# Optimization experiments

Measured on AMD Instinct MI355X. Metric: run time of the kernel, lower is better.

The kernel has to match this reference:

```python
import jax, jax.numpy as jnp
import numpy as np

# Config mirroring MultiHeadAttention1d(in_channels=256, n_heads=8, residual=False,
# kernel_size=1, attention_type=0) applied to 3-D inputs (B, C, N).
B, C, N, H, D = 4, 256, 2048, 8, 256  # per-head dim D = in_channels; OC = H*D = 2048
OC = H * D


def setup_inputs() -> dict:
    key = jax.random.key(0)
    ks = jax.random.split(key, 14)
    s = 1.0 / np.sqrt(C)
    f32 = jnp.float32
    inp = {
        "x": jax.random.normal(ks[0], (B, C, N), f32),
        "y": jax.random.normal(ks[1], (B, C, N), f32),
        # ConvNormActivation1d (kernel_size=1) == pointwise conv + (folded, eval-mode)
        # BatchNorm affine + ReLU. BN folds to per-channel scale g and shift beta.
        "Wq": jax.random.normal(ks[2], (OC, C), f32) * s,
        "bq": jax.random.normal(ks[3], (OC,), f32) * 0.01,
        "gq": jnp.ones((OC,), f32),
        "betaq": jnp.zeros((OC,), f32),
        "Wk": jax.random.normal(ks[4], (OC, C), f32) * s,
        "bk": jax.random.normal(ks[5], (OC,), f32) * 0.01,
        "gk": jnp.ones((OC,), f32),
        "betak": jnp.zeros((OC,), f32),
        "Wv": jax.random.normal(ks[6], (OC, C), f32) * s,
        "bv": jax.random.normal(ks[7], (OC,), f32) * 0.01,
        "gv": jnp.ones((OC,), f32),
        "betav": jnp.zeros((OC,), f32),
    }
    return inp


def _cna(W, b, g, beta, t):
    # 1x1 conv (channel GEMM) + folded-BN affine + ReLU; t: (B, C, N) -> (B, OC, N)
    z = jnp.einsum("oc,bcn->bon", W, t) + b[:, None]
    return jax.nn.relu(g[:, None] * z + beta[:, None])


def _heads(t):
    # (B, OC, N) -> (B, H, N, D); channel split matches torch.split chunks of size D
    return t.reshape(B, H, D, N).transpose(0, 1, 3, 2)


def reference(x, y, Wq, bq, gq, betaq, Wk, bk, gk, betak, Wv, bv, gv, betav):
    q = _heads(_cna(Wq, bq, gq, betaq, x))  # (B,H,N,D)
    k = _heads(_cna(Wk, bk, gk, betak, y))
    v = _heads(_cna(Wv, bv, gv, betav, y))
    energy = jnp.einsum("bhnd,bhmd->bhnm", q, k)  # bmm(Q, K^T)
    attn = jax.nn.softmax(energy, axis=-1)
    out = jnp.einsum("bhnm,bhmd->bhnd", attn, v)  # (B,H,N,D)
    # torch path: view(H,B,k,N,D).permute(1,0,3,2,4) -> (B,H,N,k=1,D);
    # squeeze(dim=2) is a no-op since N != 1.
    return out[:, :, :, None, :]  # (B, H, N, 1, D)
```

## Files before the change

### kernel.cpp

```cpp
#include <hip/hip_runtime.h>
#include <cstdint>
#include <cstddef>

typedef unsigned short u16;
typedef __attribute__((ext_vector_type(4))) float f32x4;
typedef __attribute__((ext_vector_type(8))) _Float16 f16x8;
typedef __attribute__((ext_vector_type(4))) u16   u16x4;
typedef __attribute__((ext_vector_type(8))) u16   u16x8;

#define DEV static __device__ __forceinline__
#define MFMA16(a,b,c) __builtin_amdgcn_mfma_f32_16x16x32_f16((a),(b),(c),0,0,0)

constexpr int Bc = 4, Cc = 256, Nc = 2048, Hc = 8, Dc = 256, OCc = 2048;

constexpr size_t OFF_XT = 0;
constexpr size_t OFF_YT = OFF_XT + (size_t)Bc*Nc*Cc*2;
constexpr size_t OFF_WQ = OFF_YT + (size_t)Bc*Nc*Cc*2;
constexpr size_t OFF_WK = OFF_WQ + (size_t)OCc*Cc*2;
constexpr size_t OFF_WV = OFF_WK + (size_t)OCc*Cc*2;
constexpr size_t OFF_BQ = OFF_WV + (size_t)OCc*Cc*2;
constexpr size_t OFF_BK = OFF_BQ + (size_t)OCc*4;
constexpr size_t OFF_BV = OFF_BK + (size_t)OCc*4;
constexpr size_t OFF_Q  = OFF_BV + (size_t)OCc*4;
constexpr size_t OFF_K  = OFF_Q  + (size_t)Bc*Hc*Nc*Dc*2;
constexpr size_t OFF_V  = OFF_K  + (size_t)Bc*Hc*Nc*Dc*2;

DEV u16 f2h(float x){
  _Float16 h = (_Float16)x;
  return __builtin_bit_cast(u16, h);
}

DEV void load_lds16(const void* g, void* l){
  __builtin_amdgcn_global_load_lds((const __attribute__((address_space(1))) int*)g,
                                   (__attribute__((address_space(3))) int*)l, 16, 0, 0);
}

__global__ __launch_bounds__(256) void transpose_cast(const float* __restrict__ x,
                                                      const float* __restrict__ y,
                                                      u16* __restrict__ XT,
                                                      u16* __restrict__ YT){
  __shared__ u16 tile[64][65];
  int b = blockIdx.z >> 1;
  const float* src = (blockIdx.z & 1) ? y : x;
  u16* dst = (blockIdx.z & 1) ? YT : XT;
  int n0 = blockIdx.x * 64, c0 = blockIdx.y * 64;
  int t = threadIdx.x;
#pragma unroll
  for (int i = 0; i < 16; ++i){
    int slot = i*256 + t;
    int cl = slot >> 6, nl = slot & 63;
    tile[cl][nl] = f2h(src[((size_t)b*Cc + c0 + cl)*Nc + n0 + nl]);
  }
  __syncthreads();
#pragma unroll
  for (int i = 0; i < 8; ++i){
    int slot = i*256 + t;
    int nl = slot >> 5, cl = (slot & 31)*2;
    uint32_t v = (uint32_t)tile[cl][nl] | ((uint32_t)tile[cl+1][nl] << 16);
    *(uint32_t*)(dst + ((size_t)b*Nc + n0 + nl)*Cc + c0 + cl) = v;
  }
}

__global__ __launch_bounds__(256) void prep_w(const float* __restrict__ W,
                                              const float* __restrict__ bsrc,
                                              const float* __restrict__ g,
                                              const float* __restrict__ beta,
                                              u16* __restrict__ Wo,
                                              float* __restrict__ bb){
  int idx = (blockIdx.x*256 + threadIdx.x) * 8;
  int o = idx >> 8, c = idx & 255;
  float gg = g[o];
  f32x4 a0 = *(const f32x4*)(W + idx);
  f32x4 a1 = *(const f32x4*)(W + idx + 4);
  u16x8 r;
#pragma unroll
  for (int i = 0; i < 4; ++i){ r[i] = f2h(a0[i]*gg); r[i+4] = f2h(a1[i]*gg); }
  *(u16x8*)(Wo + idx) = r;
  if (c == 0) bb[o] = gg*bsrc[o] + beta[o];
}

template<int SW>
__global__ __launch_bounds__(256, 2) void proj_gemm(const u16* __restrict__ Xt,
                                                    const u16* __restrict__ Wp,
                                                    const float* __restrict__ bb,
                                                    u16* __restrict__ outp){
  __shared__ __align__(16) char lds[32768];
  int t = threadIdx.x, w = t >> 6, l = t & 63, q = l & 15, g = l >> 4;
  int b = blockIdx.z;
  int n0 = blockIdx.x * 128, o0 = blockIdx.y * 128;
  f32x4 acc[4][4] = {};

  for (int it = 0; it < 4; ++it){
    __syncthreads();
#pragma unroll
    for (int j = 0; j < 8; ++j){
      int s = j*4 + w;
      int chunk = s >> 3;
      int off = (s & 7) * 1024;
      int row = (s & 7)*16 + (l >> 2);
      int part = l & 3;
      const char* gsrc;
      if (chunk < 2)
        gsrc = (const char*)(Wp + (size_t)(o0 + row)*Cc) + it*128 + chunk*64 + part*16;
      else
        gsrc = (const char*)(Xt + ((size_t)b*Nc + n0 + row)*Cc) + it*128 + (chunk & 1)*64 + part*16;
      load_lds16(gsrc, lds + chunk*8192 + off);
    }
    asm volatile("s_waitcnt vmcnt(0)" ::: "memory");
    __syncthreads();
#pragma unroll
    for (int kc = 0; kc < 2; ++kc){
      f16x8 fw[4], fx[4];
#pragma unroll
      for (int i = 0; i < 4; ++i){
        int wrow = (SW ? (w & 1) : (w >> 1))*64 + i*16 + q;
        int xrow = (SW ? (w >> 1) : (w & 1))*64 + i*16 + q;
        fw[i] = *(const f16x8*)(lds + kc*8192 + wrow*64 + g*16);
        fx[i] = *(const f16x8*)(lds + 16384 + kc*8192 + xrow*64 + g*16);
      }
#pragma unroll
      for (int i = 0; i < 4; ++i)
#pragma unroll
        for (int jj = 0; jj < 4; ++jj){
          if constexpr (!SW) acc[i][jj] = MFMA16(fw[i], fx[jj], acc[i][jj]);
          else               acc[i][jj] = MFMA16(fx[i], fw[jj], acc[i][jj]);
        }
    }
  }

  if constexpr (!SW) {
    f32x4 bias[4];
#pragma unroll
    for (int i = 0; i < 4; ++i) bias[i] = *(const f32x4*)(bb + o0 + (w>>1)*64 + i*16 + 4*g);
#pragma unroll
    for (int i = 0; i < 4; ++i)
#pragma unroll
      for (int jj = 0; jj < 4; ++jj){
        u16x4 pk;
#pragma unroll
        for (int r = 0; r < 4; ++r){
          float z = acc[i][jj][r] + bias[i][r];
          pk[r] = f2h(fmaxf(z, 0.f));
        }
        int o = o0 + (w>>1)*64 + i*16 + 4*g;
        int n = n0 + (w&1)*64 + jj*16 + q;
        int hh = o >> 8, d = o & 255;
        *(u16x4*)(outp + ((size_t)((b*Hc + hh)*Nc + n))*Dc + d) = pk;
      }
  } else {
    float biasv[4];
#pragma unroll
    for (int i = 0; i < 4; ++i) biasv[i] = bb[o0 + (w&1)*64 + i*16 + q];
#pragma unroll
    for (int i = 0; i < 4; ++i)
#pragma unroll
      for (int jj = 0; jj < 4; ++jj){
        u16x4 pk;
#pragma unroll
        for (int r = 0; r < 4; ++r){
          float z = acc[i][jj][r] + biasv[jj];
          pk[r] = f2h(fmaxf(z, 0.f));
        }
        int o = o0 + (w&1)*64 + jj*16 + q;
        int n = n0 + (w>>1)*64 + i*16 + 4*g;
        int hh = o >> 8, d = o & 255;
        *(u16x4*)(outp + ((size_t)((b*Hc + hh)*Dc + d))*Nc + n) = pk;
      }
  }
}

__global__ __launch_bounds__(256, 2) void attn_kernel(const u16* __restrict__ Qp,
                                                      const u16* __restrict__ Kp,
                                                      const u16* __restrict__ Vp,
                                                      float* __restrict__ outp){
  __shared__ __align__(16) char lds[32768 + 16384 + 4*2304];
  int t = threadIdx.x, w = t >> 6, l = t & 63, q = l & 15, g = l >> 4;
  int qt = blockIdx.x, h = blockIdx.y, b = blockIdx.z;
  int q0 = qt * 64;
  size_t head = (size_t)(b*Hc + h) * Nc * Dc;
  const u16* Kh = Kp + head;
  const u16* Vh = Vp + head;

  f16x8 qf[8];
  const u16* qrow = Qp + head + (size_t)(q0 + w*16 + q) * Dc;
#pragma unroll
  for (int kk = 0; kk < 8; ++kk) qf[kk] = *(const f16x8*)(qrow + kk*32 + g*8);

  f32x4 acc_o[16] = {};
  float m_run = -1e30f, l_run = 0.f;
  char* pbase = lds + 49152 + w*2304;

  for (int kv = 0; kv < 32; ++kv){
    int m0 = kv * 64;
    __syncthreads();
#pragma unroll
    for (int j = 0; j < 8; ++j){
      int row = w*16 + (l >> 2);
      const char* gsrc = (const char*)(Kh + (size_t)(m0 + row)*Dc) + j*64 + (l & 3)*16;
      load_lds16(gsrc, lds + j*4096 + w*1024);
    }
#pragma unroll
    for (int j = 0; j < 4; ++j){
      int s = j*4 + w;
      int row = s*16 + (l >> 2);
      const char* gsrc = (const char*)(Vh + (size_t)row*Nc + m0 + (l & 3)*8);
      load_lds16(gsrc, lds + 32768 + s*1024);
    }
    asm volatile("s_waitcnt vmcnt(0)" ::: "memory");
    __syncthreads();

    f32x4 s_acc[4];
#pragma unroll
    for (int mt = 0; mt < 4; ++mt){
      f32x4 a = {0.f, 0.f, 0.f, 0.f};
#pragma unroll
      for (int kk = 0; kk < 8; ++kk){
        f16x8 kf = *(const f16x8*)(lds + kk*4096 + (mt*16 + q)*64 + g*16);
        a = MFMA16(kf, qf[kk], a);
      }
      s_acc[mt] = a;
    }

    float tmax = -1e30f;
#pragma unroll
    for (int mt = 0; mt < 4; ++mt)
#pragma unroll
      for (int r = 0; r < 4; ++r) tmax = fmaxf(tmax, s_acc[mt][r]);
    tmax = fmaxf(tmax, __shfl_xor(tmax, 16));
    tmax = fmaxf(tmax, __shfl_xor(tmax, 32));
    float mnew = fmaxf(m_run, tmax);
    float scale = __expf(m_run - mnew);
    float rsum = 0.f;
#pragma unroll
    for (int mt = 0; mt < 4; ++mt){
      u16x4 pk;
#pragma unroll
      for (int r = 0; r < 4; ++r){
        float p = __expf(s_acc[mt][r] - mnew);
        rsum += p;
        pk[r] = f2h(p);
      }
      *(u16x4*)(pbase + q*144 + (mt*16 + 4*g)*2) = pk;
    }
    rsum += __shfl_xor(rsum, 16);
    rsum += __shfl_xor(rsum, 32);
    l_run = l_run * scale + rsum;
    m_run = mnew;
#pragma unroll
    for (int dt = 0; dt < 16; ++dt) acc_o[dt] *= scale;

    f16x8 pb0 = *(const f16x8*)(pbase + q*144 + g*16);
    f16x8 pb1 = *(const f16x8*)(pbase + q*144 + 64 + g*16);

#pragma unroll
    for (int dt = 0; dt < 16; ++dt){
      f16x8 vf = *(const f16x8*)(lds + 32768 + (dt*16 + q)*64 + g*16);
      acc_o[dt] = MFMA16(vf, pb0, acc_o[dt]);
    }
    __syncthreads();
#pragma unroll
    for (int j = 0; j < 4; ++j){
      int s = j*4 + w;
      int row = s*16 + (l >> 2);
      const char* gsrc = (const char*)(Vh + (size_t)row*Nc + m0 + 32 + (l & 3)*8);
      load_lds16(gsrc, lds + 32768 + s*1024);
    }
    asm volatile("s_waitcnt vmcnt(0)" ::: "memory");
    __syncthreads();
#pragma unroll
    for (int dt = 0; dt < 16; ++dt){
      f16x8 vf = *(const f16x8*)(lds + 32768 + (dt*16 + q)*64 + g*16);
      acc_o[dt] = MFMA16(vf, pb1, acc_o[dt]);
    }
  }

  float inv = 1.f / l_run;
  size_t obase = ((size_t)(b*Hc + h)*Nc + q0 + w*16 + q) * Dc;
#pragma unroll
  for (int dt = 0; dt < 16; ++dt){
    f32x4 v = acc_o[dt] * inv;
    *(f32x4*)(outp + obase + dt*16 + 4*g) = v;
  }
}

extern "C" void kernel_launch(void* const* d_in, const int* in_sizes, int n_in,
                              void* d_out, int out_size, void* d_ws, size_t ws_size,
                              hipStream_t stream){
  const float* x     = (const float*)d_in[0];
  const float* y     = (const float*)d_in[1];
  const float* Wq    = (const float*)d_in[2];
  const float* bq    = (const float*)d_in[3];
  const float* gq    = (const float*)d_in[4];
  const float* betaq = (const float*)d_in[5];
  const float* Wk    = (const float*)d_in[6];
  const float* bk    = (const float*)d_in[7];
  const float* gk    = (const float*)d_in[8];
  const float* betak = (const float*)d_in[9];
  const float* Wv    = (const float*)d_in[10];
  const float* bv    = (const float*)d_in[11];
  const float* gv    = (const float*)d_in[12];
  const float* betav = (const float*)d_in[13];
  char* ws = (char*)d_ws;
  float* outp = (float*)d_out;

  u16* XT = (u16*)(ws + OFF_XT);
  u16* YT = (u16*)(ws + OFF_YT);
  u16* WQb = (u16*)(ws + OFF_WQ);
  u16* WKb = (u16*)(ws + OFF_WK);
  u16* WVb = (u16*)(ws + OFF_WV);
  float* BQ = (float*)(ws + OFF_BQ);
  float* BK = (float*)(ws + OFF_BK);
  float* BV = (float*)(ws + OFF_BV);
  u16* Qw = (u16*)(ws + OFF_Q);
  u16* Kw = (u16*)(ws + OFF_K);
  u16* Vw = (u16*)(ws + OFF_V);

  transpose_cast<<<dim3(Nc/64, Cc/64, Bc*2), 256, 0, stream>>>(x, y, XT, YT);
  prep_w<<<dim3(OCc*Cc/2048), 256, 0, stream>>>(Wq, bq, gq, betaq, WQb, BQ);
  prep_w<<<dim3(OCc*Cc/2048), 256, 0, stream>>>(Wk, bk, gk, betak, WKb, BK);
  prep_w<<<dim3(OCc*Cc/2048), 256, 0, stream>>>(Wv, bv, gv, betav, WVb, BV);

  dim3 pg(Nc/128, OCc/128, Bc);
  proj_gemm<0><<<pg, 256, 0, stream>>>(XT, WQb, BQ, Qw);
  proj_gemm<0><<<pg, 256, 0, stream>>>(YT, WKb, BK, Kw);
  proj_gemm<1><<<pg, 256, 0, stream>>>(YT, WVb, BV, Vw);

  attn_kernel<<<dim3(Nc/64, Hc, Bc), 256, 0, stream>>>(Qw, Kw, Vw, outp);
}
```

Baseline: 304.0 us.

## Double attention query tile per wave and XOR-swizzle LDS layouts

The attention kernel now processes 128 queries per block, with each wave holding two 16-row query fragments. Every K and V fragment read from LDS therefore feeds two MFMAs, which halves K/V global and LDS traffic per query. K, V and the projection GEMM tiles are stored in LDS with XOR swizzles to cut bank conflicts on fragment reads. The cost is doubled accumulator registers (acc_o grows to 32 f32x4), which can lower occupancy or cause spills, and the block count drops by half.

Result: slower. 503.7 us (+65.7%).

```diff
diff --git a/kernel.cpp b/kernel.cpp
--- a/kernel.cpp
+++ b/kernel.cpp
@@ -88,6 +88,8 @@
   int t = threadIdx.x, w = t >> 6, l = t & 63, q = l & 15, g = l >> 4;
   int b = blockIdx.z;
   int n0 = blockIdx.x * 128, o0 = blockIdx.y * 128;
+  int fs = ((q >> 1) & 3) << 4;
+  int partg = ((l & 3) ^ ((l >> 3) & 3));
   f32x4 acc[4][4] = {};
 
   for (int it = 0; it < 4; ++it){
@@ -98,12 +100,11 @@
       int chunk = s >> 3;
       int off = (s & 7) * 1024;
       int row = (s & 7)*16 + (l >> 2);
-      int part = l & 3;
       const char* gsrc;
       if (chunk < 2)
-        gsrc = (const char*)(Wp + (size_t)(o0 + row)*Cc) + it*128 + chunk*64 + part*16;
+        gsrc = (const char*)(Wp + (size_t)(o0 + row)*Cc) + it*128 + chunk*64 + partg*16;
       else
-        gsrc = (const char*)(Xt + ((size_t)b*Nc + n0 + row)*Cc) + it*128 + (chunk & 1)*64 + part*16;
+        gsrc = (const char*)(Xt + ((size_t)b*Nc + n0 + row)*Cc) + it*128 + (chunk & 1)*64 + partg*16;
       load_lds16(gsrc, lds + chunk*8192 + off);
     }
     asm volatile("s_waitcnt vmcnt(0)" ::: "memory");
@@ -115,8 +116,8 @@
       for (int i = 0; i < 4; ++i){
         int wrow = (SW ? (w & 1) : (w >> 1))*64 + i*16 + q;
         int xrow = (SW ? (w >> 1) : (w & 1))*64 + i*16 + q;
-        fw[i] = *(const f16x8*)(lds + kc*8192 + wrow*64 + g*16);
-        fx[i] = *(const f16x8*)(lds + 16384 + kc*8192 + xrow*64 + g*16);
+        fw[i] = *(const f16x8*)(lds + kc*8192 + wrow*64 + ((g*16) ^ fs));
+        fx[i] = *(const f16x8*)(lds + 16384 + kc*8192 + xrow*64 + ((g*16) ^ fs));
       }
 #pragma unroll
       for (int i = 0; i < 4; ++i)
@@ -173,113 +174,141 @@
                                                       const u16* __restrict__ Kp,
                                                       const u16* __restrict__ Vp,
                                                       float* __restrict__ outp){
-  __shared__ __align__(16) char lds[32768 + 16384 + 4*2304];
-  int t = threadIdx.x, w = t >> 6, l = t & 63, q = l & 15, g = l >> 4;
-  int qt = blockIdx.x, h = blockIdx.y, b = blockIdx.z;
-  int q0 = qt * 64;
+  __shared__ __align__(16) char lds[32768 + 16384 + 4*4608];
+  int t = threadIdx.x, w = t >> 6, l = t & 63, q16 = l & 15, g = l >> 4;
+  int h = blockIdx.y, b = blockIdx.z;
+  int q0 = blockIdx.x * 128;
   size_t head = (size_t)(b*Hc + h) * Nc * Dc;
   const u16* Kh = Kp + head;
   const u16* Vh = Vp + head;
 
-  f16x8 qf[8];
-  const u16* qrow = Qp + head + (size_t)(q0 + w*16 + q) * Dc;
-#pragma unroll
-  for (int kk = 0; kk < 8; ++kk) qf[kk] = *(const f16x8*)(qrow + kk*32 + g*8);
-
-  f32x4 acc_o[16] = {};
-  float m_run = -1e30f, l_run = 0.f;
-  char* pbase = lds + 49152 + w*2304;
+  f16x8 qf[2][8];
+#pragma unroll
+  for (int jq = 0; jq < 2; ++jq){
+    const u16* qrow = Qp + head + (size_t)(q0 + w*32 + jq*16 + q16) * Dc;
+#pragma unroll
+    for (int kk = 0; kk < 8; ++kk) qf[jq][kk] = *(const f16x8*)(qrow + kk*32 + g*8);
+  }
+
+  f32x4 acc_o[16][2] = {};
+  float m_run[2] = {-1e30f, -1e30f}, l_run[2] = {0.f, 0.f};
+  char* pbase = lds + 49152 + w*4608;
+
+  const int swzA = (q16 & 7) << 4;
+  const int swzV = ((q16 >> 1) & 3) << 4;
+  const int gslotV = ((l & 3) ^ ((l >> 3) & 3));
 
   for (int kv = 0; kv < 32; ++kv){
     int m0 = kv * 64;
     __syncthreads();
 #pragma unroll
     for (int j = 0; j < 8; ++j){
-      int row = w*16 + (l >> 2);
-      const char* gsrc = (const char*)(Kh + (size_t)(m0 + row)*Dc) + j*64 + (l & 3)*16;
-      load_lds16(gsrc, lds + j*4096 + w*1024);
+      int ri = j*4 + w;
+      int mg = 2*ri + (l >> 5);
+      int gslot = (l & 31) ^ (mg & 7);
+      const char* gsrc = (const char*)(Kh + (size_t)(m0 + mg)*Dc + gslot*8);
+      load_lds16(gsrc, lds + ri*1024);
     }
 #pragma unroll
     for (int j = 0; j < 4; ++j){
-      int s = j*4 + w;
-      int row = s*16 + (l >> 2);
-      const char* gsrc = (const char*)(Vh + (size_t)row*Nc + m0 + (l & 3)*8);
-      load_lds16(gsrc, lds + 32768 + s*1024);
+      int ri = j*4 + w;
+      int dg = 16*ri + (l >> 2);
+      const char* gsrc = (const char*)(Vh + (size_t)dg*Nc + m0 + gslotV*8);
+      load_lds16(gsrc, lds + 32768 + ri*1024);
     }
     asm volatile("s_waitcnt vmcnt(0)" ::: "memory");
     __syncthreads();
 
-    f32x4 s_acc[4];
+    f32x4 s_acc[4][2];
 #pragma unroll
     for (int mt = 0; mt < 4; ++mt){
-      f32x4 a = {0.f, 0.f, 0.f, 0.f};
+      f32x4 a0 = {0.f,0.f,0.f,0.f}, a1 = {0.f,0.f,0.f,0.f};
 #pragma unroll
       for (int kk = 0; kk < 8; ++kk){
-        f16x8 kf = *(const f16x8*)(lds + kk*4096 + (mt*16 + q)*64 + g*16);
-        a = MFMA16(kf, qf[kk], a);
-      }
-      s_acc[mt] = a;
-    }
-
-    float tmax = -1e30f;
-#pragma unroll
-    for (int mt = 0; mt < 4; ++mt)
-#pragma unroll
-      for (int r = 0; r < 4; ++r) tmax = fmaxf(tmax, s_acc[mt][r]);
-    tmax = fmaxf(tmax, __shfl_xor(tmax, 16));
-    tmax = fmaxf(tmax, __shfl_xor(tmax, 32));
-    float mnew = fmaxf(m_run, tmax);
-    float scale = __expf(m_run - mnew);
-    float rsum = 0.f;
-#pragma unroll
-    for (int mt = 0; mt < 4; ++mt){
-      u16x4 pk;
-#pragma unroll
-      for (int r = 0; r < 4; ++r){
-        float p = __expf(s_acc[mt][r] - mnew);
-        rsum += p;
-        pk[r] = f2h(p);
-      }
-      *(u16x4*)(pbase + q*144 + (mt*16 + 4*g)*2) = pk;
-    }
-    rsum += __shfl_xor(rsum, 16);
-    rsum += __shfl_xor(rsum, 32);
-    l_run = l_run * scale + rsum;
-    m_run = mnew;
-#pragma unroll
-    for (int dt = 0; dt < 16; ++dt) acc_o[dt] *= scale;
-
-    f16x8 pb0 = *(const f16x8*)(pbase + q*144 + g*16);
-    f16x8 pb1 = *(const f16x8*)(pbase + q*144 + 64 + g*16);
-
+        f16x8 kf = *(const f16x8*)(lds + (mt*16 + q16)*512 + ((kk*64 + g*16) ^ swzA));
+        a0 = MFMA16(kf, qf[0][kk], a0);
+        a1 = MFMA16(kf, qf[1][kk], a1);
+      }
+      s_acc[mt][0] = a0; s_acc[mt][1] = a1;
+    }
+
+    float scale_[2];
+#pragma unroll
+    for (int jq = 0; jq < 2; ++jq){
+      float tmax = -1e30f;
+#pragma unroll
+      for (int mt = 0; mt < 4; ++mt)
+#pragma unroll
+        for (int r = 0; r < 4; ++r) tmax = fmaxf(tmax, s_acc[mt][jq][r]);
+      tmax = fmaxf(tmax, __shfl_xor(tmax, 16));
+      tmax = fmaxf(tmax, __shfl_xor(tmax, 32));
+      float mnew = fmaxf(m_run[jq], tmax);
+      float sc = __expf(m_run[jq] - mnew);
+      float rsum = 0.f;
+#pragma unroll
+      for (int mt = 0; mt < 4; ++mt){
+        u16x4 pk;
+#pragma unroll
+        for (int r = 0; r < 4; ++r){
+          float p = __expf(s_acc[mt][jq][r] - mnew);
+          rsum += p;
+          pk[r] = f2h(p);
+        }
+        *(u16x4*)(pbase + (jq*16 + q16)*144 + mt*32 + g*8) = pk;
+      }
+      rsum += __shfl_xor(rsum, 16);
+      rsum += __shfl_xor(rsum, 32);
+      l_run[jq] = l_run[jq]*sc + rsum;
+      m_run[jq] = mnew;
+      scale_[jq] = sc;
+    }
 #pragma unroll
     for (int dt = 0; dt < 16; ++dt){
-      f16x8 vf = *(const f16x8*)(lds + 32768 + (dt*16 + q)*64 + g*16);
-      acc_o[dt] = MFMA16(vf, pb0, acc_o[dt]);
+      acc_o[dt][0] *= scale_[0];
+      acc_o[dt][1] *= scale_[1];
+    }
+
+    {
+      f16x8 pb0 = *(const f16x8*)(pbase + (0*16 + q16)*144 + g*16);
+      f16x8 pb1 = *(const f16x8*)(pbase + (1*16 + q16)*144 + g*16);
+#pragma unroll
+      for (int dt = 0; dt < 16; ++dt){
+        f16x8 vf = *(const f16x8*)(lds + 32768 + (dt*16 + q16)*64 + ((g*16) ^ swzV));
+        acc_o[dt][0] = MFMA16(vf, pb0, acc_o[dt][0]);
+        acc_o[dt][1] = MFMA16(vf, pb1, acc_o[dt][1]);
+      }
     }
     __syncthreads();
 #pragma unroll
     for (int j = 0; j < 4; ++j){
-      int s = j*4 + w;
-      int row = s*16 + (l >> 2);
-      const char* gsrc = (const char*)(Vh + (size_t)row*Nc + m0 + 32 + (l & 3)*8);
-      load_lds16(gsrc, lds + 32768 + s*1024);
+      int ri = j*4 + w;
+      int dg = 16*ri + (l >> 2);
+      const char* gsrc = (const char*)(Vh + (size_t)dg*Nc + m0 + 32 + gslotV*8);
+      load_lds16(gsrc, lds + 32768 + ri*1024);
     }
     asm volatile("s_waitcnt vmcnt(0)" ::: "memory");
     __syncthreads();
+    {
+      f16x8 pb0 = *(const f16x8*)(pbase + (0*16 + q16)*144 + 64 + g*16);
+      f16x8 pb1 = *(const f16x8*)(pbase + (1*16 + q16)*144 + 64 + g*16);
+#pragma unroll
+      for (int dt = 0; dt < 16; ++dt){
+        f16x8 vf = *(const f16x8*)(lds + 32768 + (dt*16 + q16)*64 + ((g*16) ^ swzV));
+        acc_o[dt][0] = MFMA16(vf, pb0, acc_o[dt][0]);
+        acc_o[dt][1] = MFMA16(vf, pb1, acc_o[dt][1]);
+      }
+    }
+  }
+
+#pragma unroll
+  for (int jq = 0; jq < 2; ++jq){
+    float inv = 1.f / l_run[jq];
+    size_t obase = ((size_t)(b*Hc + h)*Nc + q0 + w*32 + jq*16 + q16) * Dc;
 #pragma unroll
     for (int dt = 0; dt < 16; ++dt){
-      f16x8 vf = *(const f16x8*)(lds + 32768 + (dt*16 + q)*64 + g*16);
-      acc_o[dt] = MFMA16(vf, pb1, acc_o[dt]);
-    }
-  }
-
-  float inv = 1.f / l_run;
-  size_t obase = ((size_t)(b*Hc + h)*Nc + q0 + w*16 + q) * Dc;
-#pragma unroll
-  for (int dt = 0; dt < 16; ++dt){
-    f32x4 v = acc_o[dt] * inv;
-    *(f32x4*)(outp + obase + dt*16 + 4*g) = v;
+      f32x4 v = acc_o[dt][jq] * inv;
+      *(f32x4*)(outp + obase + dt*16 + 4*g) = v;
+    }
   }
 }
 
@@ -325,5 +354,5 @@
   proj_gemm<0><<<pg, 256, 0, stream>>>(YT, WKb, BK, Kw);
   proj_gemm<1><<<pg, 256, 0, stream>>>(YT, WVb, BV, Vw);
 
-  attn_kernel<<<dim3(Nc/64, Hc, Bc), 256, 0, stream>>>(Qw, Kw, Vw, outp);
-}
+  attn_kernel<<<dim3(Nc/128, Hc, Bc), 256, 0, stream>>>(Qw, Kw, Vw, outp);
+}
```

## Rework attention kernel with 32x32 MFMA tiles, swizzled LDS and 2x2 wave split

Applied to the files above, without the earlier changes.

The attention kernel now splits work across a 2x2 wave grid, with each wave covering 32 queries and either half of the KV columns or half of the head dimension. It uses 32x32x16 MFMA instead of 16x16x32, and cross-wave row max, row sum and scale are exchanged through LDS. K, V and the projection GEMM tiles get XOR-swizzled LDS layouts to avoid bank conflicts. The aim is more data reuse per MFMA and fewer LDS conflicts. The cost is extra block-wide barriers per KV step and scalar, non-vectorized output stores.

Result: no change. 307.8 us (+1.2%).

```diff
diff --git a/kernel.cpp b/kernel.cpp
--- a/kernel.cpp
+++ b/kernel.cpp
@@ -4,12 +4,15 @@
 
 typedef unsigned short u16;
 typedef __attribute__((ext_vector_type(4))) float f32x4;
+typedef __attribute__((ext_vector_type(16))) float f32x16;
 typedef __attribute__((ext_vector_type(8))) _Float16 f16x8;
 typedef __attribute__((ext_vector_type(4))) u16   u16x4;
 typedef __attribute__((ext_vector_type(8))) u16   u16x8;
+typedef __attribute__((ext_vector_type(4))) int   i32x4;
 
 #define DEV static __device__ __forceinline__
 #define MFMA16(a,b,c) __builtin_amdgcn_mfma_f32_16x16x32_f16((a),(b),(c),0,0,0)
+#define MFMA32(a,b,c) __builtin_amdgcn_mfma_f32_32x32x16_f16((a),(b),(c),0,0,0)
 
 constexpr int Bc = 4, Cc = 256, Nc = 2048, Hc = 8, Dc = 256, OCc = 2048;
 
@@ -88,6 +91,8 @@
   int t = threadIdx.x, w = t >> 6, l = t & 63, q = l & 15, g = l >> 4;
   int b = blockIdx.z;
   int n0 = blockIdx.x * 128, o0 = blockIdx.y * 128;
+  int fs = ((q >> 1) & 3) << 4;
+  int partg = ((l & 3) ^ ((l >> 3) & 3));
   f32x4 acc[4][4] = {};
 
   for (int it = 0; it < 4; ++it){
@@ -98,12 +103,11 @@
       int chunk = s >> 3;
       int off = (s & 7) * 1024;
       int row = (s & 7)*16 + (l >> 2);
-      int part = l & 3;
       const char* gsrc;
       if (chunk < 2)
-        gsrc = (const char*)(Wp + (size_t)(o0 + row)*Cc) + it*128 + chunk*64 + part*16;
+        gsrc = (const char*)(Wp + (size_t)(o0 + row)*Cc) + it*128 + chunk*64 + partg*16;
       else
-        gsrc = (const char*)(Xt + ((size_t)b*Nc + n0 + row)*Cc) + it*128 + (chunk & 1)*64 + part*16;
+        gsrc = (const char*)(Xt + ((size_t)b*Nc + n0 + row)*Cc) + it*128 + (chunk & 1)*64 + partg*16;
       load_lds16(gsrc, lds + chunk*8192 + off);
     }
     asm volatile("s_waitcnt vmcnt(0)" ::: "memory");
@@ -115,8 +119,8 @@
       for (int i = 0; i < 4; ++i){
         int wrow = (SW ? (w & 1) : (w >> 1))*64 + i*16 + q;
         int xrow = (SW ? (w >> 1) : (w & 1))*64 + i*16 + q;
-        fw[i] = *(const f16x8*)(lds + kc*8192 + wrow*64 + g*16);
-        fx[i] = *(const f16x8*)(lds + 16384 + kc*8192 + xrow*64 + g*16);
+        fw[i] = *(const f16x8*)(lds + kc*8192 + wrow*64 + ((g*16) ^ fs));
+        fx[i] = *(const f16x8*)(lds + 16384 + kc*8192 + xrow*64 + ((g*16) ^ fs));
       }
 #pragma unroll
       for (int i = 0; i < 4; ++i)
@@ -173,114 +177,154 @@
                                                       const u16* __restrict__ Kp,
                                                       const u16* __restrict__ Vp,
                                                       float* __restrict__ outp){
-  __shared__ __align__(16) char lds[32768 + 16384 + 4*2304];
-  int t = threadIdx.x, w = t >> 6, l = t & 63, q = l & 15, g = l >> 4;
-  int qt = blockIdx.x, h = blockIdx.y, b = blockIdx.z;
-  int q0 = qt * 64;
+  __shared__ __align__(16) char lds[58880];
+  const int t = threadIdx.x, w = t >> 6, l = t & 63, lq = l & 31, hi = l >> 5;
+  const int wq = w & 1, wm = w >> 1;
+  const int h = blockIdx.y, b = blockIdx.z;
+  const int q0 = blockIdx.x * 64;
   size_t head = (size_t)(b*Hc + h) * Nc * Dc;
+  const u16* Qh = Qp + head;
   const u16* Kh = Kp + head;
   const u16* Vh = Vp + head;
 
-  f16x8 qf[8];
-  const u16* qrow = Qp + head + (size_t)(q0 + w*16 + q) * Dc;
-#pragma unroll
-  for (int kk = 0; kk < 8; ++kk) qf[kk] = *(const f16x8*)(qrow + kk*32 + g*8);
-
-  f32x4 acc_o[16] = {};
+  char* Kl = lds;
+  char* Vl = lds + 32768;
+  char* Px = lds + 49152;
+  float* smax = (float*)(lds + 57344);
+  float* ssum = (float*)(lds + 57856);
+  float* sscl = (float*)(lds + 58368);
+  float* slinv= (float*)(lds + 58624);
+
+  f16x8 qf[16];
+  {
+    const u16* qrow = Qh + (size_t)(q0 + wq*32 + lq) * Dc;
+#pragma unroll
+    for (int kc = 0; kc < 16; ++kc) qf[kc] = *(const f16x8*)(qrow + kc*16 + hi*8);
+  }
+
+  f32x16 acc[4] = {};
   float m_run = -1e30f, l_run = 0.f;
-  char* pbase = lds + 49152 + w*2304;
 
   for (int kv = 0; kv < 32; ++kv){
-    int m0 = kv * 64;
+    const int m0 = kv * 64;
     __syncthreads();
 #pragma unroll
     for (int j = 0; j < 8; ++j){
-      int row = w*16 + (l >> 2);
-      const char* gsrc = (const char*)(Kh + (size_t)(m0 + row)*Dc) + j*64 + (l & 3)*16;
-      load_lds16(gsrc, lds + j*4096 + w*1024);
+      int row = w*16 + j*2 + hi;
+      int gs = (l & 31) ^ (row & 7);
+      load_lds16(Kh + (size_t)(m0 + row)*Dc + gs*8, Kl + w*8192 + j*1024);
     }
 #pragma unroll
     for (int j = 0; j < 4; ++j){
-      int s = j*4 + w;
-      int row = s*16 + (l >> 2);
-      const char* gsrc = (const char*)(Vh + (size_t)row*Nc + m0 + (l & 3)*8);
-      load_lds16(gsrc, lds + 32768 + s*1024);
+      int ri = w*4 + j;
+      int rd = ri*16 + (l >> 2);
+      int gs = (l & 3) ^ (rd & 3);
+      load_lds16(Vh + (size_t)rd*Nc + m0 + gs*8, Vl + ri*1024);
     }
     asm volatile("s_waitcnt vmcnt(0)" ::: "memory");
     __syncthreads();
 
-    f32x4 s_acc[4];
-#pragma unroll
-    for (int mt = 0; mt < 4; ++mt){
-      f32x4 a = {0.f, 0.f, 0.f, 0.f};
-#pragma unroll
-      for (int kk = 0; kk < 8; ++kk){
-        f16x8 kf = *(const f16x8*)(lds + kk*4096 + (mt*16 + q)*64 + g*16);
-        a = MFMA16(kf, qf[kk], a);
-      }
-      s_acc[mt] = a;
-    }
-
-    float tmax = -1e30f;
-#pragma unroll
-    for (int mt = 0; mt < 4; ++mt)
-#pragma unroll
-      for (int r = 0; r < 4; ++r) tmax = fmaxf(tmax, s_acc[mt][r]);
-    tmax = fmaxf(tmax, __shfl_xor(tmax, 16));
+    f32x16 s = {};
+#pragma unroll
+    for (int kc = 0; kc < 16; ++kc){
+      f16x8 kf = *(const f16x8*)(Kl + (wm*32 + lq)*512 + ((kc*32 + hi*16) ^ ((l & 7) << 4)));
+      s = MFMA32(kf, qf[kc], s);
+    }
+
+    float tmax = s[0];
+#pragma unroll
+    for (int r = 1; r < 16; ++r) tmax = fmaxf(tmax, s[r]);
     tmax = fmaxf(tmax, __shfl_xor(tmax, 32));
-    float mnew = fmaxf(m_run, tmax);
+    if (!hi) smax[(wq*2 + wm)*32 + lq] = tmax;
+    __syncthreads();
+    float omax = smax[(wq*2 + (1 - wm))*32 + lq];
+    float mnew = fmaxf(m_run, fmaxf(tmax, omax));
     float scale = __expf(m_run - mnew);
+
+    float p[16];
     float rsum = 0.f;
 #pragma unroll
-    for (int mt = 0; mt < 4; ++mt){
-      u16x4 pk;
-#pragma unroll
-      for (int r = 0; r < 4; ++r){
-        float p = __expf(s_acc[mt][r] - mnew);
-        rsum += p;
-        pk[r] = f2h(p);
-      }
-      *(u16x4*)(pbase + q*144 + (mt*16 + 4*g)*2) = pk;
-    }
-    rsum += __shfl_xor(rsum, 16);
+    for (int r = 0; r < 16; ++r){ p[r] = __expf(s[r] - mnew); rsum += p[r]; }
     rsum += __shfl_xor(rsum, 32);
-    l_run = l_run * scale + rsum;
+    if (!hi){
+      ssum[(wq*2 + wm)*32 + lq] = rsum;
+      if (!wm) sscl[wq*32 + lq] = scale;
+    }
+
+    int pk[8];
+#pragma unroll
+    for (int j2 = 0; j2 < 8; ++j2)
+      pk[j2] = __builtin_bit_cast(int, __builtin_amdgcn_cvt_pkrtz(p[2*j2], p[2*j2+1]));
+    int sx[8];
+#pragma unroll
+    for (int j2 = 0; j2 < 8; ++j2) sx[j2] = __shfl_xor(pk[j2], 32);
+    i32x4 f0, f1;
+    f0[0] = hi ? sx[2] : pk[0];  f0[1] = hi ? sx[3] : pk[1];
+    f0[2] = hi ? pk[2] : sx[0];  f0[3] = hi ? pk[3] : sx[1];
+    f1[0] = hi ? sx[6] : pk[4];  f1[1] = hi ? sx[7] : pk[5];
+    f1[2] = hi ? pk[6] : sx[4];  f1[3] = hi ? pk[7] : sx[5];
+    *(i32x4*)(Px + w*2048 + l*16)        = f0;
+    *(i32x4*)(Px + w*2048 + 1024 + l*16) = f1;
+    __syncthreads();
+
+    float osum = ssum[(wq*2 + (1 - wm))*32 + lq];
+    l_run = l_run * scale + rsum + osum;
     m_run = mnew;
-#pragma unroll
-    for (int dt = 0; dt < 16; ++dt) acc_o[dt] *= scale;
-
-    f16x8 pb0 = *(const f16x8*)(pbase + q*144 + g*16);
-    f16x8 pb1 = *(const f16x8*)(pbase + q*144 + 64 + g*16);
-
-#pragma unroll
-    for (int dt = 0; dt < 16; ++dt){
-      f16x8 vf = *(const f16x8*)(lds + 32768 + (dt*16 + q)*64 + g*16);
-      acc_o[dt] = MFMA16(vf, pb0, acc_o[dt]);
-    }
+
+    float sc[16];
+#pragma unroll
+    for (int r = 0; r < 16; ++r) sc[r] = sscl[wq*32 + (r & 3) + 8*(r >> 2) + 4*hi];
+#pragma unroll
+    for (int dt = 0; dt < 4; ++dt)
+#pragma unroll
+      for (int r = 0; r < 16; ++r) acc[dt][r] *= sc[r];
+
+    i32x4 g0 = *(const i32x4*)(Px + (w ^ 2)*2048 + l*16);
+    i32x4 g1 = *(const i32x4*)(Px + (w ^ 2)*2048 + 1024 + l*16);
+    f16x8 a0 = __builtin_bit_cast(f16x8, wm ? g0 : f0);
+    f16x8 a1 = __builtin_bit_cast(f16x8, wm ? g1 : f1);
+    f16x8 a2 = __builtin_bit_cast(f16x8, wm ? f0 : g0);
+    f16x8 a3 = __builtin_bit_cast(f16x8, wm ? f1 : g1);
+
+#pragma unroll
+    for (int dt = 0; dt < 4; ++dt)
+#pragma unroll
+      for (int mcl = 0; mcl < 2; ++mcl){
+        f16x8 vf = *(const f16x8*)(Vl + (wm*128 + dt*32 + lq)*64 + (((mcl*2 + hi)*16) ^ ((l & 3) << 4)));
+        acc[dt] = MFMA32(mcl ? a1 : a0, vf, acc[dt]);
+      }
     __syncthreads();
 #pragma unroll
     for (int j = 0; j < 4; ++j){
-      int s = j*4 + w;
-      int row = s*16 + (l >> 2);
-      const char* gsrc = (const char*)(Vh + (size_t)row*Nc + m0 + 32 + (l & 3)*8);
-      load_lds16(gsrc, lds + 32768 + s*1024);
+      int ri = w*4 + j;
+      int rd = ri*16 + (l >> 2);
+      int gs = (l & 3) ^ (rd & 3);
+      load_lds16(Vh + (size_t)rd*Nc + m0 + 32 + gs*8, Vl + ri*1024);
     }
     asm volatile("s_waitcnt vmcnt(0)" ::: "memory");
     __syncthreads();
 #pragma unroll
-    for (int dt = 0; dt < 16; ++dt){
-      f16x8 vf = *(const f16x8*)(lds + 32768 + (dt*16 + q)*64 + g*16);
-      acc_o[dt] = MFMA16(vf, pb1, acc_o[dt]);
-    }
-  }
-
-  float inv = 1.f / l_run;
-  size_t obase = ((size_t)(b*Hc + h)*Nc + q0 + w*16 + q) * Dc;
-#pragma unroll
-  for (int dt = 0; dt < 16; ++dt){
-    f32x4 v = acc_o[dt] * inv;
-    *(f32x4*)(outp + obase + dt*16 + 4*g) = v;
-  }
+    for (int dt = 0; dt < 4; ++dt)
+#pragma unroll
+      for (int mcl = 0; mcl < 2; ++mcl){
+        f16x8 vf = *(const f16x8*)(Vl + (wm*128 + dt*32 + lq)*64 + (((mcl*2 + hi)*16) ^ ((l & 3) << 4)));
+        acc[dt] = MFMA32(mcl ? a3 : a2, vf, acc[dt]);
+      }
+  }
+
+  if (!hi && !wm) slinv[wq*32 + lq] = 1.f / l_run;
+  __syncthreads();
+  float li[16];
+#pragma unroll
+  for (int r = 0; r < 16; ++r) li[r] = slinv[wq*32 + (r & 3) + 8*(r >> 2) + 4*hi];
+#pragma unroll
+  for (int dt = 0; dt < 4; ++dt)
+#pragma unroll
+    for (int r = 0; r < 16; ++r){
+      int qrow_ = wq*32 + (r & 3) + 8*(r >> 2) + 4*hi;
+      int d = wm*128 + dt*32 + lq;
+      outp[head + (size_t)(q0 + qrow_)*Dc + d] = acc[dt][r] * li[r];
+    }
 }
 
 extern "C" void kernel_launch(void* const* d_in, const int* in_sizes, int n_in,
```
